# Performance work log

Hardware: AMD Instinct MI355X
Metric: run time of the kernel (lower is better)

The kernel has to match this reference:

```python
import jax, jax.numpy as jnp
from jax import lax
import numpy as np

SCALES = 3
DIR_PROFILE = [2, 3, 4]


def _gaussian_lowpass():
    ks, sigma = 5, 1.0
    ax = np.arange(-ks // 2 + 1.0, ks // 2 + 1.0)
    g = np.exp(-0.5 * np.square(ax) / sigma ** 2)
    k1 = g / g.sum()
    k2 = np.outer(k1, k1)
    k2 = k2 / k2.sum()
    return k2.astype(np.float32)  # [5, 5]


def _oriented_filter(angle, scale):
    size = 15
    sx, sy = 2.0 * scale, 0.5 * scale
    x = np.arange(-size // 2 + 1, size // 2 + 1)
    y = np.arange(-size // 2 + 1, size // 2 + 1)
    X, Y = np.meshgrid(x, y)
    Xr = X * np.cos(angle) - Y * np.sin(angle)
    Yr = X * np.sin(angle) + Y * np.cos(angle)
    k = np.exp(-0.5 * (Xr ** 2 / sx ** 2 + Yr ** 2 / sy ** 2)) * Xr / sx ** 2
    k = k - k.mean()
    n = np.linalg.norm(k)
    if n > 1e-6:
        k = k / n
    return k.astype(np.float32)  # [15, 15]


LP_FILTER = jnp.asarray(_gaussian_lowpass())[None, None]  # [1,1,5,5]
DIR_FILTERS = []  # per scale: [n_dirs, 1, 15, 15]
for _s, _lvl in enumerate(DIR_PROFILE):
    _nd = 2 ** _lvl
    _fs = np.stack([_oriented_filter(np.pi * d / _nd, _s + 1) for d in range(_nd)])
    DIR_FILTERS.append(jnp.asarray(_fs)[:, None])


def _depthwise(x, kernel):
    # x: [N, 1, H, W]; kernel: [O, 1, kh, kw]; reflect-pad 'same' cross-correlation
    kh, kw = kernel.shape[2], kernel.shape[3]
    xp = jnp.pad(x, ((0, 0), (0, 0), (kh // 2, kh // 2), (kw // 2, kw // 2)), mode='reflect')
    return lax.conv_general_dilated(xp, kernel, (1, 1), 'VALID',
                                    dimension_numbers=('NCHW', 'OIHW', 'NCHW'))


def setup_inputs() -> dict:
    key = jax.random.key(0)
    x = jax.random.normal(key, (8, 3, 384, 384), dtype=jnp.float32)
    return {"x": x}


def reference(x) -> jnp.ndarray:
    B, C, H, W = x.shape
    xc = x.reshape(B * C, 1, H, W)  # each RGB channel processed independently

    # Non-subsampled Laplacian pyramid: bandpasses + final lowpass
    bandpasses = []
    current = xc
    for _ in range(SCALES):
        lp = _depthwise(current, LP_FILTER)
        bandpasses.append(current - lp)
        current = lp

    # Directional filter bank per scale (all directions in one grouped conv)
    feats = []
    for s in range(SCALES):
        feats.append(_depthwise(bandpasses[s], DIR_FILTERS[s]))  # [B*C, 2^lvl, H, W]
    feats.append(current)  # final lowpass [B*C, 1, H, W]

    out = jnp.concatenate(feats, axis=1)  # [B*C, 29, H, W]
    return out.reshape(B, C * out.shape[1], H, W)  # [B, 87, H, W]
```

## Files before the change

kernel.cpp:

```cpp
#include <hip/hip_runtime.h>

#define HH 384
#define WW 384
#define HWSZ (HH * WW)
#define NIMG 24

__device__ __forceinline__ int refl(int i, int n) {
    if (i < 0) i = -i;
    if (i >= n) i = 2 * n - 2 - i;
    return i;
}

__device__ const float LPW[5] = {
    0.054488684549642945f, 0.24420134200323332f, 0.40261994689424746f,
    0.24420134200323332f, 0.054488684549642945f
};

constexpr double CPI = 3.141592653589793;

constexpr double cexp(double x) {
    int k = 0; double t = x;
    while (t > 0.25 || t < -0.25) { t *= 0.5; ++k; }
    double sum = 1.0, term = 1.0;
    for (int n = 1; n <= 14; ++n) { term *= t / n; sum += term; }
    for (int i = 0; i < k; ++i) sum *= sum;
    return sum;
}
constexpr double ccos(double x) {
    double sgn = 1.0;
    if (x > CPI * 0.5) { x = CPI - x; sgn = -1.0; }
    double x2 = x * x, sum = 1.0, term = 1.0;
    for (int n = 1; n <= 12; ++n) { term *= -x2 / ((2.0 * n - 1) * (2.0 * n)); sum += term; }
    return sgn * sum;
}
constexpr double csin(double x) {
    if (x > CPI * 0.5) x = CPI - x;
    double x2 = x * x, sum = x, term = x;
    for (int n = 1; n <= 12; ++n) { term *= -x2 / ((2.0 * n) * (2.0 * n + 1)); sum += term; }
    return sum;
}
constexpr double csqrt(double x) {
    if (x <= 0.0) return 0.0;
    double y = x > 1.0 ? x : 1.0;
    for (int i = 0; i < 80; ++i) y = 0.5 * (y + x / y);
    return y;
}

struct F225 { double v[225]; };

constexpr F225 make_filter(int s, int d, int nd) {
    double angle = CPI * (double)d / (double)nd;
    double scale = (double)(s + 1);
    double sx = 2.0 * scale, sy = 0.5 * scale;
    double ca = ccos(angle), sa = csin(angle);
    F225 f{};
    double sum = 0.0;
    for (int r = 0; r < 15; ++r)
        for (int c = 0; c < 15; ++c) {
            double X = (double)(c - 7), Y = (double)(r - 7);
            double Xr = X * ca - Y * sa;
            double Yr = X * sa + Y * ca;
            double k = cexp(-0.5 * (Xr * Xr / (sx * sx) + Yr * Yr / (sy * sy))) * Xr / (sx * sx);
            f.v[r * 15 + c] = k; sum += k;
        }
    double mean = sum / 225.0;
    double ss = 0.0;
    for (int i = 0; i < 225; ++i) { f.v[i] -= mean; ss += f.v[i] * f.v[i]; }
    double n = csqrt(ss);
    if (n > 1e-6) for (int i = 0; i < 225; ++i) f.v[i] /= n;
    return f;
}

template <int S, int D>
struct Filt { static constexpr F225 v = make_filter(S, D, S == 0 ? 4 : (S == 1 ? 8 : 16)); };

constexpr const F225& getF(int s, int d) {
    if (s == 0) {
        if (d == 0) return Filt<0, 0>::v;
        if (d == 1) return Filt<0, 1>::v;
        return Filt<0, 2>::v;
    } else if (s == 1) {
        if (d == 0) return Filt<1, 0>::v;
        if (d == 1) return Filt<1, 1>::v;
        if (d == 2) return Filt<1, 2>::v;
        if (d == 3) return Filt<1, 3>::v;
        return Filt<1, 4>::v;
    } else {
        if (d == 0) return Filt<2, 0>::v;
        if (d == 1) return Filt<2, 1>::v;
        if (d == 2) return Filt<2, 2>::v;
        if (d == 3) return Filt<2, 3>::v;
        if (d == 4) return Filt<2, 4>::v;
        if (d == 5) return Filt<2, 5>::v;
        if (d == 6) return Filt<2, 6>::v;
        if (d == 7) return Filt<2, 7>::v;
        return Filt<2, 8>::v;
    }
}

template <int NH> struct PTab { float a[63 * NH]; float b[63 * NH]; };

template <int NH>
constexpr PTab<NH> make_ptab(int s) {
    PTab<NH> t{};
    for (int j = 0; j < 63; ++j) {
        int u, v;
        if (j < 7)       { u = 0;     v = j + 1; }
        else if (j < 14) { u = j - 6; v = 0;     }
        else { int p = j - 14; u = p / 7 + 1; v = p % 7 + 1; }
        for (int k = 0; k < NH; ++k) {
            int dP = (k == 0) ? NH : k;
            int dQ = (k == 0) ? 0 : k;
            const F225& FP = getF(s, dP);
            const F225& FQ = getF(s, dQ);
            double A = 0.5 * (FP.v[(7 + u) * 15 + (7 + v)] + FP.v[(7 + u) * 15 + (7 - v)]);
            double B = 0.5 * (FQ.v[(7 + u) * 15 + (7 + v)] - FQ.v[(7 + u) * 15 + (7 - v)]);
            t.a[j * NH + k] = (float)A;
            t.b[j * NH + k] = (float)B;
        }
    }
    return t;
}
template <int S, int NH>
struct PTbl { static constexpr PTab<NH> t = make_ptab<NH>(S); };

__global__ __launch_bounds__(256, 4) void lp_fused(
    const float* __restrict__ in, float* __restrict__ lp0g,
    float* __restrict__ lp1g, float* __restrict__ outall) {
    __shared__ float sIN[44][48];
    __shared__ float sA[44][40];
    __shared__ float sB[40][40];

    int n = blockIdx.z;
    int bx = blockIdx.x * 32, by = blockIdx.y * 32;
    int tid = threadIdx.y * 32 + threadIdx.x;
    int yy = threadIdx.y, xx = threadIdx.x;
    const float* ip = in + (long)n * HWSZ;

    for (int l = tid; l < 44 * 44; l += 256) {
        int r = l / 44, c = l % 44;
        sIN[r][c] = ip[(long)refl(by + r - 6, HH) * WW + refl(bx + c - 6, WW)];
    }
    __syncthreads();
    for (int l = tid; l < 44 * 40; l += 256) {
        int r = l / 40, c = l % 40;
        float s = 0.f;
#pragma unroll
        for (int i = 0; i < 5; ++i) s = fmaf(LPW[i], sIN[r][c + i], s);
        sA[r][c] = s;
    }
    __syncthreads();
    for (int l = tid; l < 40 * 40; l += 256) {
        int r = l / 40, c = l % 40;
        float s = 0.f;
#pragma unroll
        for (int i = 0; i < 5; ++i) s = fmaf(LPW[i], sA[r + i][c], s);
        sB[r][c] = s;
    }
    __syncthreads();
    {
        float* l0 = lp0g + (long)n * HWSZ;
#pragma unroll
        for (int rr = 0; rr < 4; ++rr)
            l0[(long)(by + yy + rr * 8) * WW + bx + xx] = sB[yy + rr * 8 + 4][xx + 4];
        float* h1 = &sIN[0][0];
        for (int l = tid; l < 40 * 36; l += 256) {
            int r = l / 36, c = l % 36;
            float s = 0.f;
#pragma unroll
            for (int i = 0; i < 5; ++i) s = fmaf(LPW[i], sB[r][c + i], s);
            h1[r * 36 + c] = s;
        }
    }
    __syncthreads();
    {
        const float* h1 = &sIN[0][0];
        for (int l = tid; l < 36 * 36; l += 256) {
            int r = l / 36, c = l % 36;
            float s = 0.f;
#pragma unroll
            for (int i = 0; i < 5; ++i) s = fmaf(LPW[i], h1[(r + i) * 36 + c], s);
            sB[r][c] = s;
        }
    }
    __syncthreads();
    {
        float* l1 = lp1g + (long)n * HWSZ;
#pragma unroll
        for (int rr = 0; rr < 4; ++rr)
            l1[(long)(by + yy + rr * 8) * WW + bx + xx] = sB[yy + rr * 8 + 2][xx + 2];
        float* h2 = &sA[0][0];
        for (int l = tid; l < 36 * 32; l += 256) {
            int r = l / 32, c = l % 32;
            float s = 0.f;
#pragma unroll
            for (int i = 0; i < 5; ++i) s = fmaf(LPW[i], sB[r][c + i], s);
            h2[r * 32 + c] = s;
        }
    }
    __syncthreads();
    {
        const float* h2 = &sA[0][0];
#pragma unroll
        for (int rr = 0; rr < 4; ++rr) {
            int r = yy + rr * 8;
            float s = 0.f;
#pragma unroll
            for (int i = 0; i < 5; ++i) s = fmaf(LPW[i], h2[(r + i) * 32 + xx], s);
            outall[((long)n * 29 + 28) * HWSZ + (long)(by + r) * WW + bx + xx] = s;
        }
    }
}

template <int SIDX, int NH, int R, int U>
struct UStep {
    static __device__ __forceinline__ void run(
        const float (&sm)[8 * R + 14][48], int ty, int xc,
        float (&accP)[NH][R], float (&accQ)[NH][R]) {
        {
            float dvc[R];
#pragma unroll
            for (int r = 0; r < R; ++r) {
                int yb = ty + 7 + 8 * r;
                dvc[r] = sm[yb + U][xc] - sm[yb - U][xc];
            }
#pragma unroll
            for (int k = 0; k < NH; ++k) {
                const float cs = PTbl<SIDX, NH>::t.a[(6 + U) * NH + k];
#pragma unroll
                for (int r = 0; r < R; ++r)
                    accP[k][r] = fmaf(cs, dvc[r], accP[k][r]);
            }
        }
#pragma unroll
        for (int v = 1; v <= 7; ++v) {
            float S[R], D[R];
#pragma unroll
            for (int r = 0; r < R; ++r) {
                int yb = ty + 7 + 8 * r;
                float a = sm[yb + U][xc + v];
                float b = sm[yb + U][xc - v];
                float c = sm[yb - U][xc + v];
                float d = sm[yb - U][xc - v];
                float t1 = a - d, t2 = b - c;
                S[r] = t1 + t2;
                D[r] = t1 - t2;
            }
#pragma unroll
            for (int k = 0; k < NH; ++k) {
                const float cs = PTbl<SIDX, NH>::t.a[(14 + (U - 1) * 7 + (v - 1)) * NH + k];
                const float ca = PTbl<SIDX, NH>::t.b[(14 + (U - 1) * 7 + (v - 1)) * NH + k];
#pragma unroll
                for (int r = 0; r < R; ++r) {
                    accP[k][r] = fmaf(cs, S[r], accP[k][r]);
                    accQ[k][r] = fmaf(ca, D[r], accQ[k][r]);
                }
            }
        }
        asm volatile("" ::: "memory");
        UStep<SIDX, NH, R, U + 1>::run(sm, ty, xc, accP, accQ);
    }
};
template <int SIDX, int NH, int R>
struct UStep<SIDX, NH, R, 8> {
    static __device__ __forceinline__ void run(
        const float (&)[8 * R + 14][48], int, int,
        float (&)[NH][R], float (&)[NH][R]) {}
};

template <int SIDX, int NH, int R>
__global__ __launch_bounds__(256, 4) void dir_kernel(
    const float* __restrict__ A, long as,
    const float* __restrict__ B, long bs,
    float* __restrict__ out, int c0) {
    constexpr int TH = 8 * R;
    __shared__ float sm[TH + 14][48];

    int n = blockIdx.z;
    int tx = threadIdx.x, ty = threadIdx.y;
    int bx = blockIdx.x * 32, by = blockIdx.y * TH;

    const float* Ab = A + (long)n * as;
    const float* Bb = B + (long)n * bs;

    int lid = ty * 32 + tx;
    for (int l = lid; l < (TH + 14) * 46; l += 256) {
        int ly = l / 46, lx = l % 46;
        int gy = refl(by + ly - 7, HH);
        int gx = refl(bx + lx - 7, WW);
        long gi = (long)gy * WW + gx;
        sm[ly][lx] = Ab[gi] - Bb[gi];
    }
    __syncthreads();

    float accP[NH][R], accQ[NH][R];
#pragma unroll
    for (int k = 0; k < NH; ++k)
#pragma unroll
        for (int r = 0; r < R; ++r) { accP[k][r] = 0.f; accQ[k][r] = 0.f; }

    int xc = tx + 7;

#pragma unroll
    for (int v = 1; v <= 7; ++v) {
        float dv[R];
#pragma unroll
        for (int r = 0; r < R; ++r) {
            int yb = ty + 7 + 8 * r;
            dv[r] = sm[yb][xc + v] - sm[yb][xc - v];
        }
#pragma unroll
        for (int k = 0; k < NH; ++k) {
            const float ca = PTbl<SIDX, NH>::t.b[(v - 1) * NH + k];
#pragma unroll
            for (int r = 0; r < R; ++r)
                accQ[k][r] = fmaf(ca, dv[r], accQ[k][r]);
        }
    }
    asm volatile("" ::: "memory");

    UStep<SIDX, NH, R, 1>::run(sm, ty, xc, accP, accQ);

    long ob = ((long)n * 29 + c0) * HWSZ;
#pragma unroll
    for (int r = 0; r < R; ++r) {
        long idx = ob + (long)(by + ty + r * 8) * WW + bx + tx;
        out[idx] = accQ[0][r];
        out[idx + (long)NH * HWSZ] = accP[0][r];
#pragma unroll
        for (int k = 1; k < NH; ++k) {
            out[idx + (long)k * HWSZ] = accP[k][r] + accQ[k][r];
            out[idx + (long)(2 * NH - k) * HWSZ] = accP[k][r] - accQ[k][r];
        }
    }
}

extern "C" void kernel_launch(void* const* d_in, const int* in_sizes, int n_in,
                              void* d_out, int out_size, void* d_ws, size_t ws_size,
                              hipStream_t stream) {
    const float* x = (const float*)d_in[0];
    float* out = (float*)d_out;
    float* ws = (float*)d_ws;

    float* lp0 = ws;
    float* lp1 = lp0 + (long)NIMG * HWSZ;

    dim3 blk(32, 8);
    lp_fused<<<dim3(12, 12, NIMG), blk, 0, stream>>>(x, lp0, lp1, out);

    dir_kernel<0, 2, 4><<<dim3(12, 12, NIMG), blk, 0, stream>>>(
        x, HWSZ, lp0, HWSZ, out, 0);
    dir_kernel<1, 4, 4><<<dim3(12, 12, NIMG), blk, 0, stream>>>(
        lp0, HWSZ, lp1, HWSZ, out, 4);
    dir_kernel<2, 8, 2><<<dim3(12, 24, NIMG), blk, 0, stream>>>(
        lp1, HWSZ, out + 28l * HWSZ, 29l * HWSZ, out, 12);
}
```

Before: 605.0 us.

## Fuse lowpass pyramid and all directional filter stages into one kernel

Replaces the four launches (lowpass pyramid plus three directional kernels) with one kernel that loads a 58x58 haloed tile, computes the three lowpass levels and the bandpass differences in shared memory, and runs each directional bank from shared memory. This removes the global lp0/lp1 workspace round trips and the re-reading of inputs by each directional kernel. In exchange, larger halos cause redundant lowpass recomputation per tile, shared memory use rises (about 38 KB per block, which may limit occupancy), and the directional loops now process one row per iteration (rolled loop) instead of register-blocked multi-row accumulation. LPW is also made constexpr so its taps become compile-time constants.

After: 594.2 us. Within noise of the previous version (-1.8%).

```diff
diff --git a/kernel.cpp b/kernel.cpp
--- a/kernel.cpp
+++ b/kernel.cpp
@@ -11,7 +11,7 @@
     return i;
 }
 
-__device__ const float LPW[5] = {
+constexpr float LPW[5] = {
     0.054488684549642945f, 0.24420134200323332f, 0.40261994689424746f,
     0.24420134200323332f, 0.054488684549642945f
 };
@@ -124,215 +124,163 @@
 template <int S, int NH>
 struct PTbl { static constexpr PTab<NH> t = make_ptab<NH>(S); };
 
-__global__ __launch_bounds__(256, 4) void lp_fused(
-    const float* __restrict__ in, float* __restrict__ lp0g,
-    float* __restrict__ lp1g, float* __restrict__ outall) {
-    __shared__ float sIN[44][48];
-    __shared__ float sA[44][40];
-    __shared__ float sB[40][40];
+template <int SIDX, int NH, int U>
+struct UStep {
+    static __device__ __forceinline__ void run(
+        const float* sm, int yb, int xc, float (&accP)[NH], float (&accQ)[NH]) {
+        {
+            float dvc = sm[(yb + U) * 48 + xc] - sm[(yb - U) * 48 + xc];
+#pragma unroll
+            for (int k = 0; k < NH; ++k)
+                accP[k] = fmaf(PTbl<SIDX, NH>::t.a[(6 + U) * NH + k], dvc, accP[k]);
+        }
+#pragma unroll
+        for (int v = 1; v <= 7; ++v) {
+            float a_ = sm[(yb + U) * 48 + xc + v];
+            float b_ = sm[(yb + U) * 48 + xc - v];
+            float c_ = sm[(yb - U) * 48 + xc + v];
+            float d_ = sm[(yb - U) * 48 + xc - v];
+            float t1 = a_ - d_, t2 = b_ - c_;
+            float S = t1 + t2, D = t1 - t2;
+#pragma unroll
+            for (int k = 0; k < NH; ++k) {
+                accP[k] = fmaf(PTbl<SIDX, NH>::t.a[(14 + (U - 1) * 7 + (v - 1)) * NH + k], S, accP[k]);
+                accQ[k] = fmaf(PTbl<SIDX, NH>::t.b[(14 + (U - 1) * 7 + (v - 1)) * NH + k], D, accQ[k]);
+            }
+        }
+        asm volatile("" ::: "memory");
+        UStep<SIDX, NH, U + 1>::run(sm, yb, xc, accP, accQ);
+    }
+};
+template <int SIDX, int NH>
+struct UStep<SIDX, NH, 8> {
+    static __device__ __forceinline__ void run(
+        const float*, int, int, float (&)[NH], float (&)[NH]) {}
+};
+
+template <int SIDX, int NH>
+__device__ __forceinline__ void dir_band(
+    const float* sm, float* __restrict__ out, long nbase,
+    int by, int bx, int tx, int ty, int c0) {
+#pragma unroll 1
+    for (int rr = 0; rr < 4; ++rr) {
+        int yb = ty + 8 * rr + 7, xc = tx + 7;
+        float accP[NH], accQ[NH];
+#pragma unroll
+        for (int k = 0; k < NH; ++k) { accP[k] = 0.f; accQ[k] = 0.f; }
+
+#pragma unroll
+        for (int v = 1; v <= 7; ++v) {
+            float dv = sm[yb * 48 + xc + v] - sm[yb * 48 + xc - v];
+#pragma unroll
+            for (int k = 0; k < NH; ++k)
+                accQ[k] = fmaf(PTbl<SIDX, NH>::t.b[(v - 1) * NH + k], dv, accQ[k]);
+        }
+        asm volatile("" ::: "memory");
+
+        UStep<SIDX, NH, 1>::run(sm, yb, xc, accP, accQ);
+
+        long idx = nbase + (long)c0 * HWSZ + (long)(by + ty + 8 * rr) * WW + bx + tx;
+        out[idx] = accQ[0];
+        out[idx + (long)NH * HWSZ] = accP[0];
+#pragma unroll
+        for (int k = 1; k < NH; ++k) {
+            out[idx + (long)k * HWSZ] = accP[k] + accQ[k];
+            out[idx + (long)(2 * NH - k) * HWSZ] = accP[k] - accQ[k];
+        }
+    }
+}
+
+__global__ __launch_bounds__(256, 4) void nsst_fused(
+    const float* __restrict__ x, float* __restrict__ out) {
+    __shared__ float Xb[58 * 60];
+    __shared__ float Tb[58 * 56];
+    __shared__ float Pb[54 * 56];
 
     int n = blockIdx.z;
     int bx = blockIdx.x * 32, by = blockIdx.y * 32;
-    int tid = threadIdx.y * 32 + threadIdx.x;
-    int yy = threadIdx.y, xx = threadIdx.x;
-    const float* ip = in + (long)n * HWSZ;
-
-    for (int l = tid; l < 44 * 44; l += 256) {
-        int r = l / 44, c = l % 44;
-        sIN[r][c] = ip[(long)refl(by + r - 6, HH) * WW + refl(bx + c - 6, WW)];
-    }
-    __syncthreads();
-    for (int l = tid; l < 44 * 40; l += 256) {
-        int r = l / 40, c = l % 40;
-        float s = 0.f;
-#pragma unroll
-        for (int i = 0; i < 5; ++i) s = fmaf(LPW[i], sIN[r][c + i], s);
-        sA[r][c] = s;
-    }
-    __syncthreads();
-    for (int l = tid; l < 40 * 40; l += 256) {
-        int r = l / 40, c = l % 40;
-        float s = 0.f;
-#pragma unroll
-        for (int i = 0; i < 5; ++i) s = fmaf(LPW[i], sA[r + i][c], s);
-        sB[r][c] = s;
-    }
-    __syncthreads();
-    {
-        float* l0 = lp0g + (long)n * HWSZ;
-#pragma unroll
-        for (int rr = 0; rr < 4; ++rr)
-            l0[(long)(by + yy + rr * 8) * WW + bx + xx] = sB[yy + rr * 8 + 4][xx + 4];
-        float* h1 = &sIN[0][0];
-        for (int l = tid; l < 40 * 36; l += 256) {
-            int r = l / 36, c = l % 36;
-            float s = 0.f;
-#pragma unroll
-            for (int i = 0; i < 5; ++i) s = fmaf(LPW[i], sB[r][c + i], s);
-            h1[r * 36 + c] = s;
-        }
-    }
-    __syncthreads();
-    {
-        const float* h1 = &sIN[0][0];
-        for (int l = tid; l < 36 * 36; l += 256) {
-            int r = l / 36, c = l % 36;
-            float s = 0.f;
-#pragma unroll
-            for (int i = 0; i < 5; ++i) s = fmaf(LPW[i], h1[(r + i) * 36 + c], s);
-            sB[r][c] = s;
-        }
-    }
-    __syncthreads();
-    {
-        float* l1 = lp1g + (long)n * HWSZ;
-#pragma unroll
-        for (int rr = 0; rr < 4; ++rr)
-            l1[(long)(by + yy + rr * 8) * WW + bx + xx] = sB[yy + rr * 8 + 2][xx + 2];
-        float* h2 = &sA[0][0];
-        for (int l = tid; l < 36 * 32; l += 256) {
-            int r = l / 32, c = l % 32;
-            float s = 0.f;
-#pragma unroll
-            for (int i = 0; i < 5; ++i) s = fmaf(LPW[i], sB[r][c + i], s);
-            h2[r * 32 + c] = s;
-        }
-    }
-    __syncthreads();
-    {
-        const float* h2 = &sA[0][0];
-#pragma unroll
-        for (int rr = 0; rr < 4; ++rr) {
-            int r = yy + rr * 8;
-            float s = 0.f;
-#pragma unroll
-            for (int i = 0; i < 5; ++i) s = fmaf(LPW[i], h2[(r + i) * 32 + xx], s);
-            outall[((long)n * 29 + 28) * HWSZ + (long)(by + r) * WW + bx + xx] = s;
-        }
-    }
-}
-
-template <int SIDX, int NH, int R, int U>
-struct UStep {
-    static __device__ __forceinline__ void run(
-        const float (&sm)[8 * R + 14][48], int ty, int xc,
-        float (&accP)[NH][R], float (&accQ)[NH][R]) {
-        {
-            float dvc[R];
-#pragma unroll
-            for (int r = 0; r < R; ++r) {
-                int yb = ty + 7 + 8 * r;
-                dvc[r] = sm[yb + U][xc] - sm[yb - U][xc];
-            }
-#pragma unroll
-            for (int k = 0; k < NH; ++k) {
-                const float cs = PTbl<SIDX, NH>::t.a[(6 + U) * NH + k];
-#pragma unroll
-                for (int r = 0; r < R; ++r)
-                    accP[k][r] = fmaf(cs, dvc[r], accP[k][r]);
-            }
-        }
-#pragma unroll
-        for (int v = 1; v <= 7; ++v) {
-            float S[R], D[R];
-#pragma unroll
-            for (int r = 0; r < R; ++r) {
-                int yb = ty + 7 + 8 * r;
-                float a = sm[yb + U][xc + v];
-                float b = sm[yb + U][xc - v];
-                float c = sm[yb - U][xc + v];
-                float d = sm[yb - U][xc - v];
-                float t1 = a - d, t2 = b - c;
-                S[r] = t1 + t2;
-                D[r] = t1 - t2;
-            }
-#pragma unroll
-            for (int k = 0; k < NH; ++k) {
-                const float cs = PTbl<SIDX, NH>::t.a[(14 + (U - 1) * 7 + (v - 1)) * NH + k];
-                const float ca = PTbl<SIDX, NH>::t.b[(14 + (U - 1) * 7 + (v - 1)) * NH + k];
-#pragma unroll
-                for (int r = 0; r < R; ++r) {
-                    accP[k][r] = fmaf(cs, S[r], accP[k][r]);
-                    accQ[k][r] = fmaf(ca, D[r], accQ[k][r]);
-                }
-            }
-        }
-        asm volatile("" ::: "memory");
-        UStep<SIDX, NH, R, U + 1>::run(sm, ty, xc, accP, accQ);
-    }
-};
-template <int SIDX, int NH, int R>
-struct UStep<SIDX, NH, R, 8> {
-    static __device__ __forceinline__ void run(
-        const float (&)[8 * R + 14][48], int, int,
-        float (&)[NH][R], float (&)[NH][R]) {}
-};
-
-template <int SIDX, int NH, int R>
-__global__ __launch_bounds__(256, 4) void dir_kernel(
-    const float* __restrict__ A, long as,
-    const float* __restrict__ B, long bs,
-    float* __restrict__ out, int c0) {
-    constexpr int TH = 8 * R;
-    __shared__ float sm[TH + 14][48];
-
-    int n = blockIdx.z;
     int tx = threadIdx.x, ty = threadIdx.y;
-    int bx = blockIdx.x * 32, by = blockIdx.y * TH;
-
-    const float* Ab = A + (long)n * as;
-    const float* Bb = B + (long)n * bs;
-
-    int lid = ty * 32 + tx;
-    for (int l = lid; l < (TH + 14) * 46; l += 256) {
-        int ly = l / 46, lx = l % 46;
-        int gy = refl(by + ly - 7, HH);
-        int gx = refl(bx + lx - 7, WW);
-        long gi = (long)gy * WW + gx;
-        sm[ly][lx] = Ab[gi] - Bb[gi];
-    }
-    __syncthreads();
-
-    float accP[NH][R], accQ[NH][R];
-#pragma unroll
-    for (int k = 0; k < NH; ++k)
-#pragma unroll
-        for (int r = 0; r < R; ++r) { accP[k][r] = 0.f; accQ[k][r] = 0.f; }
-
-    int xc = tx + 7;
-
-#pragma unroll
-    for (int v = 1; v <= 7; ++v) {
-        float dv[R];
-#pragma unroll
-        for (int r = 0; r < R; ++r) {
-            int yb = ty + 7 + 8 * r;
-            dv[r] = sm[yb][xc + v] - sm[yb][xc - v];
-        }
-#pragma unroll
-        for (int k = 0; k < NH; ++k) {
-            const float ca = PTbl<SIDX, NH>::t.b[(v - 1) * NH + k];
-#pragma unroll
-            for (int r = 0; r < R; ++r)
-                accQ[k][r] = fmaf(ca, dv[r], accQ[k][r]);
-        }
-    }
-    asm volatile("" ::: "memory");
-
-    UStep<SIDX, NH, R, 1>::run(sm, ty, xc, accP, accQ);
-
-    long ob = ((long)n * 29 + c0) * HWSZ;
-#pragma unroll
-    for (int r = 0; r < R; ++r) {
-        long idx = ob + (long)(by + ty + r * 8) * WW + bx + tx;
-        out[idx] = accQ[0][r];
-        out[idx + (long)NH * HWSZ] = accP[0][r];
-#pragma unroll
-        for (int k = 1; k < NH; ++k) {
-            out[idx + (long)k * HWSZ] = accP[k][r] + accQ[k][r];
-            out[idx + (long)(2 * NH - k) * HWSZ] = accP[k][r] - accQ[k][r];
-        }
-    }
+    int tid = ty * 32 + tx;
+    const float* ip = x + (long)n * HWSZ;
+    long nbase = (long)n * 29 * HWSZ;
+
+    for (int l = tid; l < 58 * 58; l += 256) {
+        int r = l / 58, c = l % 58;
+        Xb[r * 60 + c] = ip[(long)refl(by + r - 13, HH) * WW + refl(bx + c - 13, WW)];
+    }
+    __syncthreads();
+    for (int l = tid; l < 58 * 54; l += 256) {
+        int r = l / 54, c = l % 54;
+        float s = 0.f;
+#pragma unroll
+        for (int i = 0; i < 5; ++i) s = fmaf(LPW[i], Xb[r * 60 + c + i], s);
+        Tb[r * 56 + c] = s;
+    }
+    __syncthreads();
+    for (int l = tid; l < 54 * 54; l += 256) {
+        int r = l / 54, c = l % 54;
+        float s = 0.f;
+#pragma unroll
+        for (int i = 0; i < 5; ++i) s = fmaf(LPW[i], Tb[(r + i) * 56 + c], s);
+        Pb[r * 56 + c] = s;
+    }
+    __syncthreads();
+    for (int l = tid; l < 46 * 46; l += 256) {
+        int r = l / 46, c = l % 46;
+        Tb[r * 48 + c] = Xb[(r + 6) * 60 + c + 6] - Pb[(r + 4) * 56 + c + 4];
+    }
+    __syncthreads();
+    dir_band<0, 2>(Tb, out, nbase, by, bx, tx, ty, 0);
+    __syncthreads();
+    for (int l = tid; l < 54 * 50; l += 256) {
+        int r = l / 50, c = l % 50;
+        float s = 0.f;
+#pragma unroll
+        for (int i = 0; i < 5; ++i) s = fmaf(LPW[i], Pb[r * 56 + c + i], s);
+        Tb[r * 52 + c] = s;
+    }
+    __syncthreads();
+    for (int l = tid; l < 50 * 50; l += 256) {
+        int r = l / 50, c = l % 50;
+        float s = 0.f;
+#pragma unroll
+        for (int i = 0; i < 5; ++i) s = fmaf(LPW[i], Tb[(r + i) * 52 + c], s);
+        Xb[r * 52 + c] = s;
+    }
+    __syncthreads();
+    for (int l = tid; l < 46 * 46; l += 256) {
+        int r = l / 46, c = l % 46;
+        Tb[r * 48 + c] = Pb[(r + 4) * 56 + c + 4] - Xb[(r + 2) * 52 + c + 2];
+    }
+    __syncthreads();
+    dir_band<1, 4>(Tb, out, nbase, by, bx, tx, ty, 4);
+    __syncthreads();
+    for (int l = tid; l < 50 * 46; l += 256) {
+        int r = l / 46, c = l % 46;
+        float s = 0.f;
+#pragma unroll
+        for (int i = 0; i < 5; ++i) s = fmaf(LPW[i], Xb[r * 52 + c + i], s);
+        Tb[r * 48 + c] = s;
+    }
+    __syncthreads();
+    for (int l = tid; l < 46 * 46; l += 256) {
+        int r = l / 46, c = l % 46;
+        float s = 0.f;
+#pragma unroll
+        for (int i = 0; i < 5; ++i) s = fmaf(LPW[i], Tb[(r + i) * 48 + c], s);
+        Pb[r * 48 + c] = s;
+    }
+    __syncthreads();
+#pragma unroll
+    for (int rr = 0; rr < 4; ++rr)
+        out[nbase + 28l * HWSZ + (long)(by + ty + 8 * rr) * WW + bx + tx] =
+            Pb[(ty + 8 * rr + 7) * 48 + tx + 7];
+    for (int l = tid; l < 46 * 46; l += 256) {
+        int r = l / 46, c = l % 46;
+        Tb[r * 48 + c] = Xb[(r + 2) * 52 + c + 2] - Pb[r * 48 + c];
+    }
+    __syncthreads();
+    dir_band<2, 8>(Tb, out, nbase, by, bx, tx, ty, 12);
 }
 
 extern "C" void kernel_launch(void* const* d_in, const int* in_sizes, int n_in,
@@ -340,18 +288,7 @@
                               hipStream_t stream) {
     const float* x = (const float*)d_in[0];
     float* out = (float*)d_out;
-    float* ws = (float*)d_ws;
-
-    float* lp0 = ws;
-    float* lp1 = lp0 + (long)NIMG * HWSZ;
-
-    dim3 blk(32, 8);
-    lp_fused<<<dim3(12, 12, NIMG), blk, 0, stream>>>(x, lp0, lp1, out);
-
-    dir_kernel<0, 2, 4><<<dim3(12, 12, NIMG), blk, 0, stream>>>(
-        x, HWSZ, lp0, HWSZ, out, 0);
-    dir_kernel<1, 4, 4><<<dim3(12, 12, NIMG), blk, 0, stream>>>(
-        lp0, HWSZ, lp1, HWSZ, out, 4);
-    dir_kernel<2, 8, 2><<<dim3(12, 24, NIMG), blk, 0, stream>>>(
-        lp1, HWSZ, out + 28l * HWSZ, 29l * HWSZ, out, 12);
-}
+    (void)d_ws; (void)ws_size;
+
+    nsst_fused<<<dim3(12, 12, NIMG), dim3(32, 8), 0, stream>>>(x, out);
+}
```
